# Kernel tuning notes

Measured on AMD Instinct MI355X. Metric: run time of the kernel, lower is better.

Reference implementation:

```python
import jax, jax.numpy as jnp
import numpy as np

N_NODES = 100000
N_EDGES = 3200000
D_FEAT = 256
UNITS = 256


def setup_inputs() -> dict:
    key = jax.random.key(0)
    k1, k2, k3, k4, k5 = jax.random.split(key, 5)
    X = jax.random.normal(k1, (N_NODES, D_FEAT), dtype=jnp.float32)
    edge_row = jax.random.randint(k2, (N_EDGES,), 0, N_NODES, dtype=jnp.int64 if jax.config.read('jax_enable_x64') else jnp.int32)
    edge_col = jax.random.randint(k3, (N_EDGES,), 0, N_NODES, dtype=edge_row.dtype)
    edge_val = jax.random.uniform(k4, (N_EDGES,), dtype=jnp.float32)
    W = jax.random.normal(k5, (D_FEAT, UNITS), dtype=jnp.float32) * (1.0 / np.sqrt(D_FEAT))
    b = jnp.zeros((UNITS,), dtype=jnp.float32)
    return {"X": X, "edge_row": edge_row, "edge_col": edge_col,
            "edge_val": edge_val, "W": W, "b": b}


def reference(X, edge_row, edge_col, edge_val, W, b):
    # h = X @ W  (dense GEMM)  [N, units]
    h = X @ W
    # out = A @ h (sparse COO SpMM): out[i] = sum_e val[e] * h[col[e]] for row[e]==i
    msgs = edge_val[:, None] * h[edge_col]          # [E, units] gather + scale
    out = jax.ops.segment_sum(msgs, edge_row, num_segments=X.shape[0])
    out = out + b                                    # bias_add
    return jax.nn.relu(out)                          # activation
```

## Files before the change

### kernel.cpp

```cpp
#include <hip/hip_runtime.h>
#include <hip/hip_bf16.h>

#define N_NODES 100000
#define N_EDGES 3200000
#define D_FEAT  256
#define UNITS   256

#define BROWS   128
#define NB      782
#define NCHUNK  256
#define EPB     (N_EDGES / NCHUNK)
#define MAXB    6144
#define GEMMB   ((N_NODES + 127) / 128)

using frag_ab = __attribute__((ext_vector_type(8))) short;
using frag_cd = __attribute__((ext_vector_type(4))) float;

__device__ __forceinline__ unsigned short f2bf(float f) {
    union { float f; unsigned int i; } c; c.f = f;
    unsigned int r = c.i + 0x7FFF + ((c.i >> 16) & 1);
    return (unsigned short)(r >> 16);
}

__global__ __launch_bounds__(256) void convert_wt(const float* __restrict__ W,
                                                  unsigned short* __restrict__ Wt) {
    const int n = blockIdx.x, k = threadIdx.x;
    Wt[n * 256 + k] = f2bf(W[k * 256 + n]);
}

__global__ __launch_bounds__(512) void gemm_hist(const float* __restrict__ X,
                                                 const unsigned short* __restrict__ Wt,
                                                 unsigned char* __restrict__ hq,
                                                 float* __restrict__ hscale,
                                                 const int* __restrict__ erow,
                                                 int* __restrict__ hist_g) {
    __shared__ __align__(16) unsigned char smem[32768];
    __shared__ int rowmax_i[128];
    const int t = threadIdx.x;

    if (blockIdx.x >= GEMMB) {
        int* h = (int*)smem;
        const int b = blockIdx.x - GEMMB;
        for (int i = t; i < NB; i += 512) h[i] = 0;
        __syncthreads();
        const int base_e = b * EPB;
        for (int i = t; i < EPB; i += 512)
            atomicAdd(&h[erow[base_e + i] >> 7], 1);
        __syncthreads();
        for (int i = t; i < NB; i += 512)
            hist_g[b * NB + i] = h[i];
        return;
    }

    unsigned short* As = (unsigned short*)smem;
    unsigned short* Bs = (unsigned short*)(smem + 8192);
    unsigned char*  qbuf = smem;

    const int lane = t & 63;
    const int wave = t >> 6;
    const int wm   = (wave >> 2) * 64;
    const int wn   = (wave & 3) * 64;
    const int rowBase = blockIdx.x * 128;
    const int lr = lane & 15, lq = lane >> 4;

    if (t < 128) rowmax_i[t] = 0;

    frag_cd acc[4][4];
    #pragma unroll
    for (int i = 0; i < 4; ++i)
        #pragma unroll
        for (int j = 0; j < 4; ++j)
            acc[i][j] = (frag_cd){0.f, 0.f, 0.f, 0.f};

    for (int k0 = 0; k0 < D_FEAT; k0 += 32) {
        #pragma unroll
        for (int cc = 0; cc < 2; ++cc) {
            const int c = t + cc * 512;
            const int r = c >> 3, fo = (c & 7) * 4;
            const int grow = min(rowBase + r, N_NODES - 1);
            const float4 xv = *(const float4*)(X + (size_t)grow * D_FEAT + k0 + fo);
            ushort4 o;
            o.x = f2bf(xv.x); o.y = f2bf(xv.y); o.z = f2bf(xv.z); o.w = f2bf(xv.w);
            *(ushort4*)(As + r * 32 + fo) = o;
        }
        #pragma unroll
        for (int cc = 0; cc < 2; ++cc) {
            const int c = t + cc * 512;
            *(uint4*)(Bs + c * 8) =
                *(const uint4*)(Wt + (size_t)(c >> 2) * 256 + k0 + (c & 3) * 8);
        }
        __syncthreads();

        frag_ab a[4], b[4];
        #pragma unroll
        for (int i = 0; i < 4; ++i)
            a[i] = *(const frag_ab*)(As + (wm + i * 16 + lr) * 32 + lq * 8);
        #pragma unroll
        for (int j = 0; j < 4; ++j)
            b[j] = *(const frag_ab*)(Bs + (wn + j * 16 + lr) * 32 + lq * 8);

        #pragma unroll
        for (int i = 0; i < 4; ++i)
            #pragma unroll
            for (int j = 0; j < 4; ++j)
                acc[i][j] = __builtin_amdgcn_mfma_f32_16x16x32_bf16(
                    a[i], b[j], acc[i][j], 0, 0, 0);
        __syncthreads();
    }

    float pm[4][4];
    #pragma unroll
    for (int i = 0; i < 4; ++i)
        #pragma unroll
        for (int rr = 0; rr < 4; ++rr) {
            float m = fabsf(acc[i][0][rr]);
            m = fmaxf(m, fabsf(acc[i][1][rr]));
            m = fmaxf(m, fabsf(acc[i][2][rr]));
            m = fmaxf(m, fabsf(acc[i][3][rr]));
            pm[i][rr] = m;
        }
    #pragma unroll
    for (int o = 1; o <= 8; o <<= 1)
        #pragma unroll
        for (int i = 0; i < 4; ++i)
            #pragma unroll
            for (int rr = 0; rr < 4; ++rr)
                pm[i][rr] = fmaxf(pm[i][rr], __shfl_xor(pm[i][rr], o));
    if (lr == 0) {
        #pragma unroll
        for (int i = 0; i < 4; ++i)
            #pragma unroll
            for (int rr = 0; rr < 4; ++rr)
                atomicMax(&rowmax_i[wm + i * 16 + lq * 4 + rr],
                          __float_as_int(pm[i][rr]));
    }
    __syncthreads();

    #pragma unroll
    for (int i = 0; i < 4; ++i)
        #pragma unroll
        for (int rr = 0; rr < 4; ++rr) {
            const int row = wm + i * 16 + lq * 4 + rr;
            const float m = __int_as_float(rowmax_i[row]);
            const float inv = (m > 0.f) ? 127.f / m : 0.f;
            #pragma unroll
            for (int j = 0; j < 4; ++j) {
                const int q = (int)rintf(acc[i][j][rr] * inv);
                qbuf[row * 256 + wn + j * 16 + lr] = (unsigned char)(signed char)q;
            }
        }
    __syncthreads();

    #pragma unroll
    for (int cc = 0; cc < 4; ++cc) {
        const int c = t + cc * 512;
        const int row = c >> 4, fo = (c & 15) * 16;
        const int grow = rowBase + row;
        if (grow < N_NODES)
            *(uint4*)(hq + (size_t)grow * 256 + fo) = *(const uint4*)(qbuf + row * 256 + fo);
    }
    if (t < 128 && rowBase + t < N_NODES)
        hscale[rowBase + t] = __int_as_float(rowmax_i[t]) * (1.f / 127.f);
}

__global__ __launch_bounds__(256) void scan_buckets(const int* __restrict__ hist_g,
                                                    int* __restrict__ cum,
                                                    int* __restrict__ total) {
    const int k = blockIdx.x, t = threadIdx.x;
    __shared__ int p[256];
    const int v = hist_g[t * NB + k];
    p[t] = v;
    __syncthreads();
    for (int d = 1; d < 256; d <<= 1) {
        const int u = (t >= d) ? p[t - d] : 0;
        __syncthreads();
        p[t] += u;
        __syncthreads();
    }
    cum[t * NB + k] = p[t] - v;
    if (t == 255) total[k] = p[255];
}

__global__ __launch_bounds__(1024) void scan_base(const int* __restrict__ total,
                                                  int* __restrict__ base) {
    const int t = threadIdx.x;
    __shared__ int p[1024];
    const int v = (t < NB) ? total[t] : 0;
    p[t] = v;
    __syncthreads();
    for (int d = 1; d < 1024; d <<= 1) {
        const int u = (t >= d) ? p[t - d] : 0;
        __syncthreads();
        p[t] += u;
        __syncthreads();
    }
    if (t < NB) base[t] = p[t] - v;
    if (t == NB - 1) base[NB] = p[t];
}

__global__ __launch_bounds__(256) void scatter_binned(const int* __restrict__ erow,
                                                      const int* __restrict__ ecol,
                                                      const float* __restrict__ eval,
                                                      const float* __restrict__ hscale,
                                                      const int* __restrict__ cum,
                                                      const int* __restrict__ base,
                                                      uint2* __restrict__ binned) {
    __shared__ int cur[NB];
    const int t = threadIdx.x;
    const int b = blockIdx.x;
    for (int i = t; i < NB; i += 256)
        cur[i] = base[i] + cum[b * NB + i];
    __syncthreads();
    const int base_e = b * EPB;
    for (int i = t; i < EPB; i += 256) {
        const int e = base_e + i;
        const int r = erow[e];
        const int c = ecol[e];
        const float v = eval[e] * hscale[c];
        const int k = r >> 7, rl = r & 127;
        const int pos = atomicAdd(&cur[k], 1);
        binned[pos] = make_uint2(((unsigned)rl << 17) | (unsigned)c,
                                 __float_as_uint(v));
    }
}

__global__ __launch_bounds__(256) void sort_local(const uint2* __restrict__ binned,
                                                  const int* __restrict__ base,
                                                  const int* __restrict__ total,
                                                  uint2* __restrict__ sorted,
                                                  int* __restrict__ offs) {
    __shared__ uint2 buf[MAXB];
    __shared__ int lh[BROWS], loff[BROWS], lcur[BROWS];
    const int k = blockIdx.x, t = threadIdx.x;
    const int s = base[k];
    const int cnt = min(total[k], MAXB);

    if (t < BROWS) lh[t] = 0;
    __syncthreads();
    for (int i = t; i < cnt; i += 256)
        atomicAdd(&lh[binned[s + i].x >> 17], 1);
    __syncthreads();
    if (t < BROWS) loff[t] = lh[t];
    __syncthreads();
    for (int d = 1; d < BROWS; d <<= 1) {
        const int u = (t >= d && t < BROWS) ? loff[t - d] : 0;
        __syncthreads();
        if (t < BROWS) loff[t] += u;
        __syncthreads();
    }
    if (t < BROWS) lcur[t] = loff[t] - lh[t];
    __syncthreads();
    for (int i = t; i < cnt; i += 256) {
        const uint2 eo = binned[s + i];
        const int rl = eo.x >> 17;
        const int p = atomicAdd(&lcur[rl], 1);
        buf[p] = make_uint2(eo.x & 0x1FFFF, eo.y);
    }
    __syncthreads();
    for (int i = t; i < cnt; i += 256)
        sorted[s + i] = buf[i];
    const int rowBase = k * BROWS;
    if (t < BROWS && rowBase + t < N_NODES)
        offs[rowBase + t] = s + (loff[t] - lh[t]);
    if (t == 0 && k == NB - 1)
        offs[N_NODES] = N_EDGES;
}

__global__ __launch_bounds__(64) void spmm_rows(const int* __restrict__ offs,
                                                const uint2* __restrict__ sorted,
                                                const unsigned char* __restrict__ hq,
                                                const float* __restrict__ bias,
                                                float* __restrict__ out) {
    const int r = blockIdx.x;
    const int lane = threadIdx.x;
    __shared__ uint2 le[64];
    int s = offs[r];
    const int e = offs[r + 1];
    float a0 = 0.f, a1 = 0.f, a2 = 0.f, a3 = 0.f;

    while (s < e) {
        const int cnt = min(64, e - s);
        if (lane < cnt) {
            uint2 v = sorted[s + lane];
            v.x &= 0x1FFFF;
            le[lane] = v;
        }
        __syncthreads();
        #pragma unroll 4
        for (int j = 0; j < cnt; ++j) {
            const uint2 cv = le[j];
            const float v = __uint_as_float(cv.y);
            const unsigned int w = *(const unsigned int*)(hq + (size_t)cv.x * 256 + lane * 4);
            a0 += v * (float)((int)(signed char)( w        & 0xFF));
            a1 += v * (float)((int)(signed char)((w >> 8)  & 0xFF));
            a2 += v * (float)((int)(signed char)((w >> 16) & 0xFF));
            a3 += v * (float)((int)(signed char)( w >> 24        ));
        }
        __syncthreads();
        s += cnt;
    }

    const float4 b4 = *(const float4*)(bias + lane * 4);
    float4 o;
    o.x = fmaxf(a0 + b4.x, 0.f);
    o.y = fmaxf(a1 + b4.y, 0.f);
    o.z = fmaxf(a2 + b4.z, 0.f);
    o.w = fmaxf(a3 + b4.w, 0.f);
    *(float4*)(out + (size_t)r * 256 + lane * 4) = o;
}

extern "C" void kernel_launch(void* const* d_in, const int* in_sizes, int n_in,
                              void* d_out, int out_size, void* d_ws, size_t ws_size,
                              hipStream_t stream) {
    const float* X    = (const float*)d_in[0];
    const int*   erow = (const int*)  d_in[1];
    const int*   ecol = (const int*)  d_in[2];
    const float* evalv= (const float*)d_in[3];
    const float* W    = (const float*)d_in[4];
    const float* bias = (const float*)d_in[5];
    float* out = (float*)d_out;

    char* ws = (char*)d_ws;
    size_t off = 0;
    auto alloc = [&](size_t bytes) {
        void* p = ws + off;
        off += (bytes + 255) & ~(size_t)255;
        return p;
    };
    unsigned short* Wt     = (unsigned short*)alloc((size_t)D_FEAT * UNITS * 2);
    unsigned char*  hq     = (unsigned char*) alloc((size_t)N_NODES * UNITS);
    float*          hscale = (float*)         alloc((size_t)N_NODES * 4);
    uint2*          binned = (uint2*)         alloc((size_t)N_EDGES * 8);
    uint2*          sorted = (uint2*)         alloc((size_t)N_EDGES * 8);
    int*            hist_g = (int*)           alloc((size_t)NCHUNK * NB * 4);
    int*            cum    = (int*)           alloc((size_t)NCHUNK * NB * 4);
    int*            total  = (int*)           alloc((size_t)NB * 4);
    int*            basep  = (int*)           alloc((size_t)(NB + 1) * 4);
    int*            offs   = (int*)           alloc((size_t)(N_NODES + 1) * 4);

    convert_wt<<<UNITS, 256, 0, stream>>>(W, Wt);
    gemm_hist<<<GEMMB + NCHUNK, 512, 0, stream>>>(X, Wt, hq, hscale, erow, hist_g);
    scan_buckets<<<NB, 256, 0, stream>>>(hist_g, cum, total);
    scan_base<<<1, 1024, 0, stream>>>(total, basep);
    scatter_binned<<<NCHUNK, 256, 0, stream>>>(erow, ecol, evalv, hscale, cum, basep, binned);
    sort_local<<<NB, 256, 0, stream>>>(binned, basep, total, sorted, offs);
    spmm_rows<<<N_NODES, 64, 0, stream>>>(offs, sorted, hq, bias, out);
}
```

Measured before the change: 436.1 us.

## Fuse local bucket sort with SpMM, consuming sorted edges from LDS

Merges the per-bucket counting sort and the row-wise SpMM into one kernel with 512 threads per block. Edges are loaded once into registers, sorted into shared memory, and each wave then accumulates 16 rows directly from the shared buffer. This removes the global sorted array and the row offsets array, along with their writes and reads and one launch. In exchange, parallelism in the gather phase drops from one block per row to 782 larger blocks, which can limit latency hiding.

```diff
diff --git a/kernel.cpp b/kernel.cpp
--- a/kernel.cpp
+++ b/kernel.cpp
@@ -11,6 +11,7 @@
 #define NCHUNK  256
 #define EPB     (N_EDGES / NCHUNK)
 #define MAXB    6144
+#define KPT     (MAXB / 512)
 #define GEMMB   ((N_NODES + 127) / 128)
 
 using frag_ab = __attribute__((ext_vector_type(8))) short;
@@ -224,21 +225,31 @@
     }
 }
 
-__global__ __launch_bounds__(256) void sort_local(const uint2* __restrict__ binned,
-                                                  const int* __restrict__ base,
-                                                  const int* __restrict__ total,
-                                                  uint2* __restrict__ sorted,
-                                                  int* __restrict__ offs) {
+__global__ __launch_bounds__(512) void sort_spmm(const uint2* __restrict__ binned,
+                                                 const int* __restrict__ base,
+                                                 const int* __restrict__ total,
+                                                 const unsigned char* __restrict__ hq,
+                                                 const float* __restrict__ bias,
+                                                 float* __restrict__ out) {
     __shared__ uint2 buf[MAXB];
     __shared__ int lh[BROWS], loff[BROWS], lcur[BROWS];
     const int k = blockIdx.x, t = threadIdx.x;
     const int s = base[k];
     const int cnt = min(total[k], MAXB);
 
+    uint2 ed[KPT];
+    #pragma unroll
+    for (int kk = 0; kk < KPT; ++kk) {
+        const int i = t + kk * 512;
+        if (i < cnt) ed[kk] = binned[s + i];
+    }
+
     if (t < BROWS) lh[t] = 0;
     __syncthreads();
-    for (int i = t; i < cnt; i += 256)
-        atomicAdd(&lh[binned[s + i].x >> 17], 1);
+    #pragma unroll
+    for (int kk = 0; kk < KPT; ++kk)
+        if (t + kk * 512 < cnt)
+            atomicAdd(&lh[ed[kk].x >> 17], 1);
     __syncthreads();
     if (t < BROWS) loff[t] = lh[t];
     __syncthreads();
@@ -250,45 +261,30 @@
     }
     if (t < BROWS) lcur[t] = loff[t] - lh[t];
     __syncthreads();
-    for (int i = t; i < cnt; i += 256) {
-        const uint2 eo = binned[s + i];
-        const int rl = eo.x >> 17;
-        const int p = atomicAdd(&lcur[rl], 1);
-        buf[p] = make_uint2(eo.x & 0x1FFFF, eo.y);
-    }
-    __syncthreads();
-    for (int i = t; i < cnt; i += 256)
-        sorted[s + i] = buf[i];
+
+    #pragma unroll
+    for (int kk = 0; kk < KPT; ++kk) {
+        if (t + kk * 512 < cnt) {
+            const int rl = ed[kk].x >> 17;
+            const int p = atomicAdd(&lcur[rl], 1);
+            buf[p] = make_uint2(ed[kk].x & 0x1FFFF, ed[kk].y);
+        }
+    }
+    __syncthreads();
+
+    const int wave = t >> 6, lane = t & 63;
     const int rowBase = k * BROWS;
-    if (t < BROWS && rowBase + t < N_NODES)
-        offs[rowBase + t] = s + (loff[t] - lh[t]);
-    if (t == 0 && k == NB - 1)
-        offs[N_NODES] = N_EDGES;
-}
-
-__global__ __launch_bounds__(64) void spmm_rows(const int* __restrict__ offs,
-                                                const uint2* __restrict__ sorted,
-                                                const unsigned char* __restrict__ hq,
-                                                const float* __restrict__ bias,
-                                                float* __restrict__ out) {
-    const int r = blockIdx.x;
-    const int lane = threadIdx.x;
-    __shared__ uint2 le[64];
-    int s = offs[r];
-    const int e = offs[r + 1];
-    float a0 = 0.f, a1 = 0.f, a2 = 0.f, a3 = 0.f;
-
-    while (s < e) {
-        const int cnt = min(64, e - s);
-        if (lane < cnt) {
-            uint2 v = sorted[s + lane];
-            v.x &= 0x1FFFF;
-            le[lane] = v;
-        }
-        __syncthreads();
+    const float4 b4 = *(const float4*)(bias + lane * 4);
+
+    for (int rr = 0; rr < 16; ++rr) {
+        const int rl = wave * 16 + rr;
+        const int gr = rowBase + rl;
+        const int je = loff[rl];
+        int j = je - lh[rl];
+        float a0 = 0.f, a1 = 0.f, a2 = 0.f, a3 = 0.f;
         #pragma unroll 4
-        for (int j = 0; j < cnt; ++j) {
-            const uint2 cv = le[j];
+        for (; j < je; ++j) {
+            const uint2 cv = buf[j];
             const float v = __uint_as_float(cv.y);
             const unsigned int w = *(const unsigned int*)(hq + (size_t)cv.x * 256 + lane * 4);
             a0 += v * (float)((int)(signed char)( w        & 0xFF));
@@ -296,17 +292,15 @@
             a2 += v * (float)((int)(signed char)((w >> 16) & 0xFF));
             a3 += v * (float)((int)(signed char)( w >> 24        ));
         }
-        __syncthreads();
-        s += cnt;
-    }
-
-    const float4 b4 = *(const float4*)(bias + lane * 4);
-    float4 o;
-    o.x = fmaxf(a0 + b4.x, 0.f);
-    o.y = fmaxf(a1 + b4.y, 0.f);
-    o.z = fmaxf(a2 + b4.z, 0.f);
-    o.w = fmaxf(a3 + b4.w, 0.f);
-    *(float4*)(out + (size_t)r * 256 + lane * 4) = o;
+        if (gr < N_NODES) {
+            float4 o;
+            o.x = fmaxf(a0 + b4.x, 0.f);
+            o.y = fmaxf(a1 + b4.y, 0.f);
+            o.z = fmaxf(a2 + b4.z, 0.f);
+            o.w = fmaxf(a3 + b4.w, 0.f);
+            *(float4*)(out + (size_t)gr * 256 + lane * 4) = o;
+        }
+    }
 }
 
 extern "C" void kernel_launch(void* const* d_in, const int* in_sizes, int n_in,
@@ -331,18 +325,15 @@
     unsigned char*  hq     = (unsigned char*) alloc((size_t)N_NODES * UNITS);
     float*          hscale = (float*)         alloc((size_t)N_NODES * 4);
     uint2*          binned = (uint2*)         alloc((size_t)N_EDGES * 8);
-    uint2*          sorted = (uint2*)         alloc((size_t)N_EDGES * 8);
     int*            hist_g = (int*)           alloc((size_t)NCHUNK * NB * 4);
     int*            cum    = (int*)           alloc((size_t)NCHUNK * NB * 4);
     int*            total  = (int*)           alloc((size_t)NB * 4);
     int*            basep  = (int*)           alloc((size_t)(NB + 1) * 4);
-    int*            offs   = (int*)           alloc((size_t)(N_NODES + 1) * 4);
 
     convert_wt<<<UNITS, 256, 0, stream>>>(W, Wt);
     gemm_hist<<<GEMMB + NCHUNK, 512, 0, stream>>>(X, Wt, hq, hscale, erow, hist_g);
     scan_buckets<<<NB, 256, 0, stream>>>(hist_g, cum, total);
     scan_base<<<1, 1024, 0, stream>>>(total, basep);
     scatter_binned<<<NCHUNK, 256, 0, stream>>>(erow, ecol, evalv, hscale, cum, basep, binned);
-    sort_local<<<NB, 256, 0, stream>>>(binned, basep, total, sorted, offs);
-    spmm_rows<<<N_NODES, 64, 0, stream>>>(offs, sorted, hq, bias, out);
-}
+    sort_spmm<<<NB, 512, 0, stream>>>(binned, basep, total, hq, bias, out);
+}
```

Result: slower. 478.5 us (+9.7%).
